# Optimization experiments

Hardware: AMD Instinct MI355X
Metric: run time of the kernel (lower is better)

Reference implementation:

```python
import jax, jax.numpy as jnp
import numpy as np
import math

B, S, D, H = 4, 2048, 1024, 16
DEPTH = D // H


def setup_inputs() -> dict:
    key = jax.random.key(0)
    ks = jax.random.split(key, 8)
    scale = 1.0 / math.sqrt(D)
    return {
        "v": jax.random.normal(ks[0], (B, S, D), dtype=jnp.float32),
        "k": jax.random.normal(ks[1], (B, S, D), dtype=jnp.float32),
        "q": jax.random.normal(ks[2], (B, S, D), dtype=jnp.float32),
        "wq_w": jax.random.normal(ks[3], (D, D), dtype=jnp.float32) * scale,
        "wq_b": jnp.zeros((D,), dtype=jnp.float32),
        "wk_w": jax.random.normal(ks[4], (D, D), dtype=jnp.float32) * scale,
        "wk_b": jnp.zeros((D,), dtype=jnp.float32),
        "wv_w": jax.random.normal(ks[5], (D, D), dtype=jnp.float32) * scale,
        "wv_b": jnp.zeros((D,), dtype=jnp.float32),
        "dense_w": jax.random.normal(ks[6], (D, D), dtype=jnp.float32) * scale,
        "dense_b": jnp.zeros((D,), dtype=jnp.float32),
    }


def _split_heads(x):
    # [B, S, D] -> [B, H, S, depth]
    b, s, _ = x.shape
    return x.reshape(b, s, H, DEPTH).transpose(0, 2, 1, 3)


def reference(v, k, q, wq_w, wq_b, wk_w, wk_b, wv_w, wv_b, dense_w, dense_b):
    # Linear projections (torch Linear: x @ W.T + b)
    qh = _split_heads(q @ wq_w.T + wq_b)
    kh = _split_heads(k @ wk_w.T + wk_b)
    vh = _split_heads(v @ wv_w.T + wv_b)

    # scaled dot-product attention; scores: [B, H, S, S]
    scores = jnp.einsum("bhqd,bhkd->bhqk", qh, kh) / math.sqrt(DEPTH)
    attn = jax.nn.softmax(scores, axis=-1)
    ctx = jnp.einsum("bhqk,bhkd->bhqd", attn, vh)

    # merge heads: [B, H, S, depth] -> [B, S, D]
    ctx = ctx.transpose(0, 2, 1, 3).reshape(q.shape[0], -1, D)
    return ctx @ dense_w.T + dense_b
```

## Files before the change

### kernel.cpp

```cpp
#include <hip/hip_runtime.h>
#include <hip/hip_bf16.h>
#include <stdint.h>

#define B_  4
#define S_  2048
#define D_  1024
#define H_  16
#define DP_ 64
#define M_  (B_*S_)

typedef __bf16 bf16x8 __attribute__((ext_vector_type(8)));
typedef __bf16 bf16x2_t __attribute__((ext_vector_type(2)));
typedef float  f32x4  __attribute__((ext_vector_type(4)));
typedef float  f32x2_t __attribute__((ext_vector_type(2)));
typedef unsigned short u16x8 __attribute__((ext_vector_type(8)));

__device__ __forceinline__ unsigned short f2bf(float f) {
    __bf16 b = (__bf16)f;
    return __builtin_bit_cast(unsigned short, b);
}
__device__ __forceinline__ unsigned pk_bf16(float lo, float hi) {
    f32x2_t f = {lo, hi};
    bf16x2_t b = __builtin_convertvector(f, bf16x2_t);
    return __builtin_bit_cast(unsigned, b);
}
__device__ __forceinline__ bf16x8 ld_frag(const unsigned short* p) {
    return __builtin_bit_cast(bf16x8, *(const u16x8*)p);
}
__device__ __forceinline__ f32x4 mfma16(bf16x8 a, bf16x8 b, f32x4 c) {
    return __builtin_amdgcn_mfma_f32_16x16x32_bf16(a, b, c, 0, 0, 0);
}
__device__ __forceinline__ void gl2lds16(const void* g, void* l) {
    __builtin_amdgcn_global_load_lds(
        (const __attribute__((address_space(1))) unsigned*)g,
        (__attribute__((address_space(3))) unsigned*)l, 16, 0, 0);
}

__global__ __launch_bounds__(256)
void cvt_all(const float* __restrict__ w0, const float* __restrict__ w1,
             const float* __restrict__ w2, const float* __restrict__ w3,
             const float* __restrict__ a0, const float* __restrict__ a1,
             const float* __restrict__ a2,
             unsigned short* __restrict__ Wcat, unsigned short* __restrict__ Acat)
{
    const int gid = blockIdx.x * 256 + threadIdx.x;
    const float* src; unsigned short* dst;
    if (gid < 524288) {
        const int wi = gid >> 17;
        const size_t off = (size_t)(gid & 131071) * 8;
        const float* ws[4] = {w0, w1, w2, w3};
        src = ws[wi] + off; dst = Wcat + (size_t)wi * 1048576 + off;
    } else {
        const int g2 = gid - 524288;
        const int ai = g2 >> 20;
        const size_t off = (size_t)(g2 & 1048575) * 8;
        const float* as[3] = {a0, a1, a2};
        src = as[ai] + off; dst = Acat + (size_t)ai * 8388608 + off;
    }
    float4 x = ((const float4*)src)[0];
    float4 y = ((const float4*)src)[1];
    uint4 o;
    o.x = pk_bf16(x.x, x.y); o.y = pk_bf16(x.z, x.w);
    o.z = pk_bf16(y.x, y.y); o.w = pk_bf16(y.z, y.w);
    *(uint4*)dst = o;
}

template<int MODE>
__global__ __launch_bounds__(256, 3)
void gemm_bt(const unsigned short* __restrict__ Acat, size_t a_stride,
             const unsigned short* __restrict__ Wcat,
             const float* __restrict__ bias0, const float* __restrict__ bias1,
             void* __restrict__ Out)
{
    __shared__ __align__(16) unsigned short SM[16384];
    unsigned short* As = SM;
    unsigned short* Bs = SM + 8192;

    const int z = (MODE == 1) ? blockIdx.z : 0;
    const unsigned short* A = Acat + (size_t)z * a_stride;
    const unsigned short* W = Wcat + ((size_t)z << 20);
    const float* bias = (z == 0) ? bias0 : bias1;

    const int tid  = threadIdx.x;
    const int wave = tid >> 6, lane = tid & 63;
    const int quad = lane >> 4, l16 = lane & 15;
    const int wm = (wave >> 1) * 64, wn = (wave & 1) * 64;
    const int row0 = blockIdx.x * 128, col0 = blockIdx.y * 128;

    const int srow = lane >> 3;
    const int sg   = (lane & 7) ^ srow;

    f32x4 acc[4][4];
#pragma unroll
    for (int i = 0; i < 4; i++)
#pragma unroll
        for (int j = 0; j < 4; j++) acc[i][j] = (f32x4){0.f, 0.f, 0.f, 0.f};

    auto stage = [&](int kt) {
        const int k0 = kt * 64;
#pragma unroll
        for (int j = 0; j < 4; ++j) {
            const int c = wave * 4 + j;
            gl2lds16(A + (size_t)(row0 + c * 8 + srow) * D_ + k0 + sg * 8,
                     (unsigned char*)As + c * 1024);
            gl2lds16(W + (size_t)(col0 + c * 8 + srow) * D_ + k0 + sg * 8,
                     (unsigned char*)Bs + c * 1024);
        }
    };

    stage(0);
    for (int kt = 0; kt < D_ / 64; ++kt) {
        __syncthreads();
        bf16x8 af[4][2], bv[4][2];
#pragma unroll
        for (int mi = 0; mi < 4; ++mi) {
            const int row = wm + mi * 16 + l16;
#pragma unroll
            for (int kd = 0; kd < 2; ++kd)
                af[mi][kd] = ld_frag(&As[row * 64 + (((kd * 4 + quad) ^ (row & 7)) * 8)]);
        }
#pragma unroll
        for (int ni = 0; ni < 4; ++ni) {
            const int row = wn + ni * 16 + l16;
#pragma unroll
            for (int kd = 0; kd < 2; ++kd)
                bv[ni][kd] = ld_frag(&Bs[row * 64 + (((kd * 4 + quad) ^ (row & 7)) * 8)]);
        }
        if (kt + 1 < D_ / 64) {
            __syncthreads();
            stage(kt + 1);
        }
#pragma unroll
        for (int kd = 0; kd < 2; ++kd)
#pragma unroll
            for (int mi = 0; mi < 4; ++mi)
#pragma unroll
                for (int ni = 0; ni < 4; ++ni) {
                    if (MODE == 1)
                        acc[mi][ni] = mfma16(bv[ni][kd], af[mi][kd], acc[mi][ni]);
                    else
                        acc[mi][ni] = mfma16(af[mi][kd], bv[ni][kd], acc[mi][ni]);
                }
    }

    if constexpr (MODE == 1) {
        unsigned short* Lt = SM;
        unsigned short* OutQK = (unsigned short*)Out + ((size_t)z << 23);
        const int bidx = row0 >> 11;
        const float scale = (z == 0) ? 0.18033688f : 1.0f;
#pragma unroll
        for (int hc = 0; hc < 2; ++hc) {
            __syncthreads();
            if ((wave & 1) == hc) {
#pragma unroll
                for (int ni = 0; ni < 4; ++ni) {
                    const int c_loc = wn + ni * 16 + quad * 4;
                    const float4 bb = *(const float4*)&bias[col0 + c_loc];
#pragma unroll
                    for (int mi = 0; mi < 4; ++mi) {
                        const int s_loc = wm + mi * 16 + l16;
                        uint2 w;
                        w.x = pk_bf16((acc[mi][ni][0] + bb.x) * scale,
                                      (acc[mi][ni][1] + bb.y) * scale);
                        w.y = pk_bf16((acc[mi][ni][2] + bb.z) * scale,
                                      (acc[mi][ni][3] + bb.w) * scale);
                        *(uint2*)&Lt[s_loc * 72 + (c_loc & 63)] = w;
                    }
                }
            }
            __syncthreads();
            const int hg = (col0 >> 6) + hc;
            const size_t qb = (size_t)(bidx * H_ + hg) * S_ + (row0 & (S_ - 1));
#pragma unroll
            for (int p = 0; p < 4; ++p) {
                const int s = p * 32 + (tid >> 3);
                const int g = tid & 7;
                uint4 d = *(const uint4*)&Lt[s * 72 + g * 8];
                *(uint4*)(OutQK + (qb + s) * DP_ + g * 8) = d;
            }
        }
        return;
    }
    if constexpr (MODE == 2) {
        unsigned short* Lt = SM;
        unsigned short* OutV = (unsigned short*)Out;
        const int bidx = row0 >> 11;
#pragma unroll
        for (int hc = 0; hc < 2; ++hc) {
            __syncthreads();
            if ((wave & 1) == hc) {
#pragma unroll
                for (int ni = 0; ni < 4; ++ni) {
                    const float bvv = bias0[col0 + hc * 64 + ni * 16 + l16];
#pragma unroll
                    for (int mi = 0; mi < 4; ++mi) {
                        uint2 w;
                        w.x = pk_bf16(acc[mi][ni][0] + bvv, acc[mi][ni][1] + bvv);
                        w.y = pk_bf16(acc[mi][ni][2] + bvv, acc[mi][ni][3] + bvv);
                        *(uint2*)&Lt[(ni * 16 + l16) * 132 + wm + mi * 16 + quad * 4] = w;
                    }
                }
            }
            __syncthreads();
            const int hg = (col0 >> 6) + hc;
            const size_t vb = ((size_t)(bidx * H_ + hg) * DP_) * S_;
#pragma unroll
            for (int p = 0; p < 4; ++p) {
                const int dpl = p * 16 + (tid >> 4);
                uint4 d = *(const uint4*)&Lt[dpl * 132 + (tid & 15) * 8];
                *(uint4*)(OutV + vb + (size_t)dpl * S_ + (row0 & (S_ - 1)) + (tid & 15) * 8) = d;
            }
        }
        return;
    }
#pragma unroll
    for (int ni = 0; ni < 4; ni++) {
        const int col = col0 + wn + ni * 16 + l16;
        const float bvv = bias0[col];
#pragma unroll
        for (int mi = 0; mi < 4; mi++) {
            const int rowb = row0 + wm + mi * 16 + quad * 4;
#pragma unroll
            for (int r = 0; r < 4; r++)
                ((float*)Out)[(size_t)(rowb + r) * D_ + col] = acc[mi][ni][r] + bvv;
        }
    }
}

__global__ __launch_bounds__(256)
void flash_attn(const unsigned short* __restrict__ Qh,
                const unsigned short* __restrict__ Kh,
                const unsigned short* __restrict__ Vtg,
                unsigned short* __restrict__ Ctx)
{
    constexpr int LP = 40;
    __shared__ __align__(16) unsigned short Kt[128 * 64];
    __shared__ __align__(16) unsigned short Vt[64 * 128];

    const int tid  = threadIdx.x;
    const int wave = tid >> 6, lane = tid & 63;
    const int quad = lane >> 4, l16 = lane & 15;
    const int bh = blockIdx.x, qt = blockIdx.y;
    const size_t base = (size_t)bh * S_ * DP_;

    bf16x8 qf[2][2];
#pragma unroll
    for (int mi = 0; mi < 2; mi++)
#pragma unroll
        for (int kd = 0; kd < 2; kd++)
            qf[mi][kd] = ld_frag(&Qh[base + (size_t)(qt * 128 + wave * 32 + mi * 16 + l16) * DP_ + kd * 32 + quad * 8]);

    f32x4 o[2][4];
    f32x2_t ls[2] = {(f32x2_t){0.f, 0.f}, (f32x2_t){0.f, 0.f}};
#pragma unroll
    for (int mi = 0; mi < 2; mi++)
#pragma unroll
        for (int nd = 0; nd < 4; nd++) o[mi][nd] = (f32x4){0.f, 0.f, 0.f, 0.f};

    unsigned short* pw = Kt + wave * 32 * LP;
    const int kswz = ((lane & 7) ^ (lane >> 3)) * 8;
    const int vdp_l = lane >> 4;
    const int vslot = lane & 15;

    for (int t = 0; t < S_ / 128; ++t) {
        __syncthreads();
#pragma unroll
        for (int j = 0; j < 4; ++j) {
            const int ck = wave * 4 + j;
            gl2lds16(Kh + base + (size_t)(t * 128 + ck * 8 + (lane >> 3)) * DP_ + kswz,
                     (unsigned char*)Kt + ck * 1024);
            const int dp = ck * 4 + vdp_l;
            gl2lds16(Vtg + base + (size_t)dp * S_ + t * 128 + ((vslot ^ (dp & 15)) * 8),
                     (unsigned char*)Vt + ck * 1024);
        }
        __syncthreads();

        f32x4 st[8][2];
#pragma unroll
        for (int kb = 0; kb < 8; ++kb) { st[kb][0] = (f32x4){0,0,0,0}; st[kb][1] = (f32x4){0,0,0,0}; }
        __builtin_amdgcn_s_setprio(1);
#pragma unroll
        for (int kb = 0; kb < 8; ++kb) {
            const int krow = (kb * 16 + l16) * 64;
            bf16x8 kf0 = ld_frag(&Kt[krow + (((quad)     ^ (l16 & 7)) * 8)]);
            bf16x8 kf1 = ld_frag(&Kt[krow + (((4 + quad) ^ (l16 & 7)) * 8)]);
            st[kb][0] = mfma16(kf0, qf[0][0], st[kb][0]);
            st[kb][0] = mfma16(kf1, qf[0][1], st[kb][0]);
            st[kb][1] = mfma16(kf0, qf[1][0], st[kb][1]);
            st[kb][1] = mfma16(kf1, qf[1][1], st[kb][1]);
        }
        __builtin_amdgcn_s_setprio(0);

        __syncthreads();

#pragma unroll
        for (int ch = 0; ch < 4; ++ch) {
#pragma unroll
            for (int kk = 0; kk < 2; ++kk)
#pragma unroll
                for (int mi = 0; mi < 2; ++mi) {
                    f32x4 s = st[2 * ch + kk][mi];
                    float p0 = __builtin_amdgcn_exp2f(s[0]);
                    float p1 = __builtin_amdgcn_exp2f(s[1]);
                    float p2 = __builtin_amdgcn_exp2f(s[2]);
                    float p3 = __builtin_amdgcn_exp2f(s[3]);
                    ls[mi] += (f32x2_t){p0, p2};
                    ls[mi] += (f32x2_t){p1, p3};
                    uint2 w;
                    w.x = pk_bf16(p0, p1);
                    w.y = pk_bf16(p2, p3);
                    *(uint2*)&pw[(mi * 16 + l16) * LP + kk * 16 + quad * 4] = w;
                }
            asm volatile("s_waitcnt lgkmcnt(0)" ::: "memory");
            bf16x8 pa0 = ld_frag(&pw[(l16)      * LP + quad * 8]);
            bf16x8 pa1 = ld_frag(&pw[(16 + l16) * LP + quad * 8]);
            __builtin_amdgcn_s_setprio(1);
#pragma unroll
            for (int nd = 0; nd < 4; ++nd) {
                const int dp = nd * 16 + l16;
                bf16x8 vbf = ld_frag(&Vt[dp * 128 + (((ch * 4 + quad) ^ l16) * 8)]);
                o[0][nd] = mfma16(pa0, vbf, o[0][nd]);
                o[1][nd] = mfma16(pa1, vbf, o[1][nd]);
            }
            __builtin_amdgcn_s_setprio(0);
            asm volatile("" ::: "memory");
        }
    }

    float lsum[2];
#pragma unroll
    for (int mi = 0; mi < 2; ++mi) {
        lsum[mi] = ls[mi][0] + ls[mi][1];
        lsum[mi] += __shfl_xor(lsum[mi], 16, 64);
        lsum[mi] += __shfl_xor(lsum[mi], 32, 64);
    }

    const int b = bh >> 4, h = bh & 15;
#pragma unroll
    for (int mi = 0; mi < 2; ++mi)
#pragma unroll
        for (int r = 0; r < 4; ++r) {
            const float lT  = __shfl(lsum[mi], quad * 4 + r, 64);
            const float inv = __builtin_amdgcn_rcpf(lT);
            const int srw = qt * 128 + wave * 32 + mi * 16 + quad * 4 + r;
#pragma unroll
            for (int nd = 0; nd < 4; ++nd)
                Ctx[((size_t)(b * S_ + srw)) * D_ + h * DP_ + nd * 16 + l16] = f2bf(o[mi][nd][r] * inv);
        }
}

extern "C" void kernel_launch(void* const* d_in, const int* in_sizes, int n_in,
                              void* d_out, int out_size, void* d_ws, size_t ws_size,
                              hipStream_t stream)
{
    const float* v    = (const float*)d_in[0];
    const float* k    = (const float*)d_in[1];
    const float* q    = (const float*)d_in[2];
    const float* wq_w = (const float*)d_in[3];
    const float* wq_b = (const float*)d_in[4];
    const float* wk_w = (const float*)d_in[5];
    const float* wk_b = (const float*)d_in[6];
    const float* wv_w = (const float*)d_in[7];
    const float* wv_b = (const float*)d_in[8];
    const float* dw   = (const float*)d_in[9];
    const float* db   = (const float*)d_in[10];
    float* out = (float*)d_out;

    unsigned short* Qh   = (unsigned short*)d_ws;
    unsigned short* Kh   = Qh   + (size_t)M_ * D_;
    unsigned short* Vt   = Kh   + (size_t)M_ * D_;
    unsigned short* Ctx  = Vt   + (size_t)M_ * D_;
    unsigned short* Wcat = Ctx  + (size_t)M_ * D_;
    unsigned short* Acat = Wcat + (size_t)4 * D_ * D_;

    cvt_all<<<14336, 256, 0, stream>>>(wq_w, wk_w, wv_w, dw, q, k, v, Wcat, Acat);

    dim3 blk(256);
    gemm_bt<1><<<dim3(M_ / 128, D_ / 128, 2), blk, 0, stream>>>(
        Acat, (size_t)M_ * D_, Wcat, wq_b, wk_b, Qh);
    gemm_bt<2><<<dim3(M_ / 128, D_ / 128, 1), blk, 0, stream>>>(
        Acat + (size_t)2 * M_ * D_, 0, Wcat + (size_t)2 * D_ * D_, wv_b, wv_b, Vt);

    flash_attn<<<dim3(B_ * H_, S_ / 128), blk, 0, stream>>>(Qh, Kh, Vt, Ctx);

    gemm_bt<0><<<dim3(M_ / 128, D_ / 128, 1), blk, 0, stream>>>(
        Ctx, 0, Wcat + (size_t)3 * D_ * D_, db, db, out);
}
```

Before: 350.2 us.

## Switch flash attention to 32x32 MFMA with register P and double-buffered V

Rewrites the attention inner loop to use 32x32x16 bf16 MFMA tiles in place of 16x16x32. The probability matrix P now stays in registers, rearranged with v_permlane32_swap, so the LDS round trip and its waitcnt are gone. V is double-buffered in LDS and the next tile's K/V loads are issued right after the QK^T stage, to overlap global loads with the softmax and PV compute. The cost is a larger LDS footprint and more accumulator registers, which may lower occupancy.

```diff
diff --git a/kernel.cpp b/kernel.cpp
--- a/kernel.cpp
+++ b/kernel.cpp
@@ -12,6 +12,7 @@
 typedef __bf16 bf16x8 __attribute__((ext_vector_type(8)));
 typedef __bf16 bf16x2_t __attribute__((ext_vector_type(2)));
 typedef float  f32x4  __attribute__((ext_vector_type(4)));
+typedef float  f32x16 __attribute__((ext_vector_type(16)));
 typedef float  f32x2_t __attribute__((ext_vector_type(2)));
 typedef unsigned short u16x8 __attribute__((ext_vector_type(8)));
 
@@ -29,6 +30,12 @@
 }
 __device__ __forceinline__ f32x4 mfma16(bf16x8 a, bf16x8 b, f32x4 c) {
     return __builtin_amdgcn_mfma_f32_16x16x32_bf16(a, b, c, 0, 0, 0);
+}
+__device__ __forceinline__ f32x16 mfma32(bf16x8 a, bf16x8 b, f32x16 c) {
+    return __builtin_amdgcn_mfma_f32_32x32x16_bf16(a, b, c, 0, 0, 0);
+}
+__device__ __forceinline__ void pl32swap(unsigned &a, unsigned &b) {
+    asm volatile("v_permlane32_swap_b32 %0, %1" : "+v"(a), "+v"(b));
 }
 __device__ __forceinline__ void gl2lds16(const void* g, void* l) {
     __builtin_amdgcn_global_load_lds(
@@ -233,120 +240,111 @@
                 const unsigned short* __restrict__ Vtg,
                 unsigned short* __restrict__ Ctx)
 {
-    constexpr int LP = 40;
     __shared__ __align__(16) unsigned short Kt[128 * 64];
-    __shared__ __align__(16) unsigned short Vt[64 * 128];
+    __shared__ __align__(16) unsigned short Vt[2][64 * 128];
 
     const int tid  = threadIdx.x;
     const int wave = tid >> 6, lane = tid & 63;
-    const int quad = lane >> 4, l16 = lane & 15;
+    const int l32 = lane & 31, hi = lane >> 5;
     const int bh = blockIdx.x, qt = blockIdx.y;
     const size_t base = (size_t)bh * S_ * DP_;
 
-    bf16x8 qf[2][2];
-#pragma unroll
-    for (int mi = 0; mi < 2; mi++)
-#pragma unroll
-        for (int kd = 0; kd < 2; kd++)
-            qf[mi][kd] = ld_frag(&Qh[base + (size_t)(qt * 128 + wave * 32 + mi * 16 + l16) * DP_ + kd * 32 + quad * 8]);
-
-    f32x4 o[2][4];
-    f32x2_t ls[2] = {(f32x2_t){0.f, 0.f}, (f32x2_t){0.f, 0.f}};
-#pragma unroll
-    for (int mi = 0; mi < 2; mi++)
-#pragma unroll
-        for (int nd = 0; nd < 4; nd++) o[mi][nd] = (f32x4){0.f, 0.f, 0.f, 0.f};
-
-    unsigned short* pw = Kt + wave * 32 * LP;
-    const int kswz = ((lane & 7) ^ (lane >> 3)) * 8;
+    bf16x8 qf[4];
+#pragma unroll
+    for (int dpc = 0; dpc < 4; ++dpc)
+        qf[dpc] = ld_frag(&Qh[base + (size_t)(qt * 128 + wave * 32 + l32) * DP_ + dpc * 16 + hi * 8]);
+
+    f32x16 o[2] = {};
+    f32x2_t ls = {0.f, 0.f};
+
+    const int kswz  = ((lane & 7) ^ (lane >> 3)) * 8;
     const int vdp_l = lane >> 4;
     const int vslot = lane & 15;
 
-    for (int t = 0; t < S_ / 128; ++t) {
-        __syncthreads();
+    auto stageK = [&](int t) {
 #pragma unroll
         for (int j = 0; j < 4; ++j) {
             const int ck = wave * 4 + j;
             gl2lds16(Kh + base + (size_t)(t * 128 + ck * 8 + (lane >> 3)) * DP_ + kswz,
                      (unsigned char*)Kt + ck * 1024);
+        }
+    };
+    auto stageV = [&](int t, unsigned short* Vb) {
+#pragma unroll
+        for (int j = 0; j < 4; ++j) {
+            const int ck = wave * 4 + j;
             const int dp = ck * 4 + vdp_l;
             gl2lds16(Vtg + base + (size_t)dp * S_ + t * 128 + ((vslot ^ (dp & 15)) * 8),
-                     (unsigned char*)Vt + ck * 1024);
-        }
+                     (unsigned char*)Vb + ck * 1024);
+        }
+    };
+
+    stageK(0); stageV(0, Vt[0]);
+
+    for (int t = 0; t < S_ / 128; ++t) {
         __syncthreads();
 
-        f32x4 st[8][2];
-#pragma unroll
-        for (int kb = 0; kb < 8; ++kb) { st[kb][0] = (f32x4){0,0,0,0}; st[kb][1] = (f32x4){0,0,0,0}; }
+        f32x16 st[4] = {};
         __builtin_amdgcn_s_setprio(1);
 #pragma unroll
-        for (int kb = 0; kb < 8; ++kb) {
-            const int krow = (kb * 16 + l16) * 64;
-            bf16x8 kf0 = ld_frag(&Kt[krow + (((quad)     ^ (l16 & 7)) * 8)]);
-            bf16x8 kf1 = ld_frag(&Kt[krow + (((4 + quad) ^ (l16 & 7)) * 8)]);
-            st[kb][0] = mfma16(kf0, qf[0][0], st[kb][0]);
-            st[kb][0] = mfma16(kf1, qf[0][1], st[kb][0]);
-            st[kb][1] = mfma16(kf0, qf[1][0], st[kb][1]);
-            st[kb][1] = mfma16(kf1, qf[1][1], st[kb][1]);
+        for (int kt = 0; kt < 4; ++kt) {
+#pragma unroll
+            for (int dpc = 0; dpc < 4; ++dpc) {
+                bf16x8 kf = ld_frag(&Kt[(kt * 32 + l32) * 64 + ((((dpc << 1) + hi) ^ (l32 & 7)) * 8)]);
+                st[kt] = mfma32(kf, qf[dpc], st[kt]);
+            }
         }
         __builtin_amdgcn_s_setprio(0);
 
         __syncthreads();
-
-#pragma unroll
-        for (int ch = 0; ch < 4; ++ch) {
-#pragma unroll
-            for (int kk = 0; kk < 2; ++kk)
-#pragma unroll
-                for (int mi = 0; mi < 2; ++mi) {
-                    f32x4 s = st[2 * ch + kk][mi];
-                    float p0 = __builtin_amdgcn_exp2f(s[0]);
-                    float p1 = __builtin_amdgcn_exp2f(s[1]);
-                    float p2 = __builtin_amdgcn_exp2f(s[2]);
-                    float p3 = __builtin_amdgcn_exp2f(s[3]);
-                    ls[mi] += (f32x2_t){p0, p2};
-                    ls[mi] += (f32x2_t){p1, p3};
-                    uint2 w;
-                    w.x = pk_bf16(p0, p1);
-                    w.y = pk_bf16(p2, p3);
-                    *(uint2*)&pw[(mi * 16 + l16) * LP + kk * 16 + quad * 4] = w;
+        if (t + 1 < S_ / 128) {
+            stageK(t + 1);
+            stageV(t + 1, Vt[(t + 1) & 1]);
+        }
+
+        const unsigned short* Vc = Vt[t & 1];
+#pragma unroll
+        for (int kt = 0; kt < 4; ++kt) {
+            float p[16];
+#pragma unroll
+            for (int r = 0; r < 16; ++r) p[r] = __builtin_amdgcn_exp2f(st[kt][r]);
+#pragma unroll
+            for (int r = 0; r < 16; r += 2) ls += (f32x2_t){p[r], p[r + 1]};
+            unsigned m[8];
+#pragma unroll
+            for (int j = 0; j < 8; ++j) m[j] = pk_bf16(p[2 * j], p[2 * j + 1]);
+            pl32swap(m[0], m[2]); pl32swap(m[1], m[3]);
+            pl32swap(m[4], m[6]); pl32swap(m[5], m[7]);
+            __builtin_amdgcn_s_setprio(1);
+#pragma unroll
+            for (int c = 0; c < 2; ++c) {
+                const bf16x8 pa = __builtin_bit_cast(bf16x8,
+                    (uint4){m[4 * c], m[4 * c + 1], m[4 * c + 2], m[4 * c + 3]});
+#pragma unroll
+                for (int nt = 0; nt < 2; ++nt) {
+                    const int dp = nt * 32 + l32;
+                    bf16x8 vb = ld_frag(&Vc[dp * 128 + ((((kt << 2) + (c << 1) + hi) ^ (dp & 15)) * 8)]);
+                    o[nt] = mfma32(pa, vb, o[nt]);
                 }
-            asm volatile("s_waitcnt lgkmcnt(0)" ::: "memory");
-            bf16x8 pa0 = ld_frag(&pw[(l16)      * LP + quad * 8]);
-            bf16x8 pa1 = ld_frag(&pw[(16 + l16) * LP + quad * 8]);
-            __builtin_amdgcn_s_setprio(1);
-#pragma unroll
-            for (int nd = 0; nd < 4; ++nd) {
-                const int dp = nd * 16 + l16;
-                bf16x8 vbf = ld_frag(&Vt[dp * 128 + (((ch * 4 + quad) ^ l16) * 8)]);
-                o[0][nd] = mfma16(pa0, vbf, o[0][nd]);
-                o[1][nd] = mfma16(pa1, vbf, o[1][nd]);
             }
             __builtin_amdgcn_s_setprio(0);
-            asm volatile("" ::: "memory");
-        }
-    }
-
-    float lsum[2];
-#pragma unroll
-    for (int mi = 0; mi < 2; ++mi) {
-        lsum[mi] = ls[mi][0] + ls[mi][1];
-        lsum[mi] += __shfl_xor(lsum[mi], 16, 64);
-        lsum[mi] += __shfl_xor(lsum[mi], 32, 64);
-    }
+        }
+    }
+
+    float lsum = ls[0] + ls[1];
+    lsum += __shfl_xor(lsum, 32, 64);
+    const float inv = __builtin_amdgcn_rcpf(lsum);
 
     const int b = bh >> 4, h = bh & 15;
 #pragma unroll
-    for (int mi = 0; mi < 2; ++mi)
-#pragma unroll
-        for (int r = 0; r < 4; ++r) {
-            const float lT  = __shfl(lsum[mi], quad * 4 + r, 64);
-            const float inv = __builtin_amdgcn_rcpf(lT);
-            const int srw = qt * 128 + wave * 32 + mi * 16 + quad * 4 + r;
-#pragma unroll
-            for (int nd = 0; nd < 4; ++nd)
-                Ctx[((size_t)(b * S_ + srw)) * D_ + h * DP_ + nd * 16 + l16] = f2bf(o[mi][nd][r] * inv);
-        }
+    for (int r = 0; r < 16; ++r) {
+        const int qrow = (r & 3) + 8 * (r >> 2) + 4 * hi;
+        const float invr = __shfl(inv, qrow, 64);
+        const int s = qt * 128 + wave * 32 + qrow;
+#pragma unroll
+        for (int nt = 0; nt < 2; ++nt)
+            Ctx[((size_t)(b * S_ + s)) * D_ + h * DP_ + nt * 32 + l32] = f2bf(o[nt][r] * invr);
+    }
 }
 
 extern "C" void kernel_launch(void* const* d_in, const int* in_sizes, int n_in,
```

Measured after the change: 331.0 us. 1.06x faster.
